# Performance work log

Hardware: AMD Instinct MI355X
Metric: run time of the kernel (lower is better)

## Reference

```python
import jax, jax.numpy as jnp
import numpy as np

B = 1 << 20
N_FREQS = 6          # sin+cos -> 3*2*6 = 36 dims for position
N_BINS = 4           # one-blob bins -> 4 dims per scalar
W_SCALE = 0.18       # ~ sqrt(2/64) He init for ReLU


def freq_embed(p):
    # p: [B,3] -> [B, 3*2*N_FREQS] NeRF-style sin/cos frequency encoding
    freqs = (2.0 ** jnp.arange(N_FREQS, dtype=p.dtype)) * jnp.pi  # [F]
    ang = p[:, :, None] * freqs  # [B,3,F]
    return jnp.concatenate([jnp.sin(ang), jnp.cos(ang)], axis=-1).reshape(p.shape[0], -1)


def one_blob_embed(x):
    # x: [B,D] values in [0,1] -> [B, D*N_BINS] Gaussian one-blob encoding
    centers = (jnp.arange(N_BINS, dtype=x.dtype) + 0.5) / N_BINS  # [K]
    sigma = 1.0 / N_BINS
    val = jnp.exp(-0.5 * ((x[:, :, None] - centers) / sigma) ** 2)  # [B,D,K]
    return val.reshape(x.shape[0], -1)


def to_sphe_coords(d):
    # unit direction [B,3] -> normalized (theta, phi) in [0,1]^2
    theta = jnp.arccos(jnp.clip(d[:, 2], -1.0, 1.0)) / jnp.pi
    phi = jnp.arctan2(d[:, 1], d[:, 0]) / (2.0 * jnp.pi) + 0.5
    return jnp.stack([theta, phi], axis=-1)


def setup_inputs() -> dict:
    key = jax.random.key(0)
    ks = jax.random.split(key, 13)
    p = jax.random.normal(ks[0], (B, 3), dtype=jnp.float32)
    wi = jax.random.normal(ks[1], (B, 3), dtype=jnp.float32)
    wi = wi / jnp.linalg.norm(wi, axis=-1, keepdims=True)
    n = jax.random.normal(ks[2], (B, 3), dtype=jnp.float32)
    n = n / jnp.linalg.norm(n, axis=-1, keepdims=True)
    alpha = jax.random.uniform(ks[3], (B, 3), dtype=jnp.float32)
    beta = jax.random.uniform(ks[4], (B, 3), dtype=jnp.float32)
    r = jax.random.uniform(ks[5], (B, 1), dtype=jnp.float32)
    Ws = {}
    for i in range(6):
        Ws[f"W{i}"] = jax.random.normal(ks[6 + i], (64, 64), dtype=jnp.float32) * W_SCALE
    Ws["W6"] = jax.random.normal(ks[12], (3, 64), dtype=jnp.float32) * W_SCALE
    return dict(p=p, wi=wi, n=n, alpha=alpha, beta=beta, r=r, **Ws)


def reference(p, wi, n, alpha, beta, r, W0, W1, W2, W3, W4, W5, W6):
    x = jnp.concatenate([
        freq_embed(p),                               # 36
        one_blob_embed(to_sphe_coords(wi)),          # 8
        one_blob_embed(to_sphe_coords(n)),           # 8
        one_blob_embed(1.0 - jnp.exp(-r)),           # 4
        alpha,                                       # 3
        beta,                                        # 3
        jnp.ones_like(p[:, :2]),                     # 2 (implicit bias)
    ], axis=-1)  # [B,64]
    h = x
    for W in (W0, W1, W2, W3, W4, W5):
        h = jax.nn.relu(h @ W.T)
    out = h @ W6.T  # [B,3]
    return out * (alpha + beta)  # reflectance factorization
```

## Files before the change

kernel.cpp:

```cpp
#include <hip/hip_runtime.h>

typedef __attribute__((ext_vector_type(8))) short short8;
typedef __attribute__((ext_vector_type(4))) float f32x4;

typedef __attribute__((address_space(3))) unsigned short lds_us;
typedef const __attribute__((address_space(1))) unsigned short glb_us;

__device__ __forceinline__ unsigned short f2bf(float x) {
  union { float f; unsigned u; } v; v.f = x;
  unsigned r = v.u + 0x7fffu + ((v.u >> 16) & 1u);
  return (unsigned short)(r >> 16);
}

#if __has_builtin(__builtin_amdgcn_cvt_pk_bf16_f32)
__device__ __forceinline__ unsigned pk2(float a, float b) {
  return __builtin_bit_cast(unsigned, __builtin_amdgcn_cvt_pk_bf16_f32(a, b));
}
#else
__device__ __forceinline__ unsigned pk2(float a, float b) {
  union { float f; unsigned u; } x, y; x.f = a; y.f = b;
  return __builtin_amdgcn_perm(y.u + 0x8000u, x.u + 0x8000u, 0x07060302u);
}
#endif

__device__ __forceinline__ unsigned relu_pk(unsigned x) {
  unsigned r;
  asm("v_pk_max_i16 %0, %1, %2" : "=v"(r) : "v"(x), "v"(0));
  return r;
}

__device__ __forceinline__ short8 u2s8(uint4 u) {
  union { uint4 a; short8 b; } c; c.a = u; return c.b;
}

__device__ __forceinline__ void wave_mem_fence() {
  asm volatile("" ::: "memory");
  __builtin_amdgcn_wave_barrier();
  asm volatile("" ::: "memory");
}

__device__ __forceinline__ void gload16(const unsigned short* g, unsigned short* l) {
  __builtin_amdgcn_global_load_lds((glb_us*)g, (lds_us*)l, 16, 0, 0);
}

__device__ __forceinline__ float acos01(float z) {
  float ax = fminf(fabsf(z), 1.0f);
  float t  = __builtin_amdgcn_sqrtf(1.0f - ax);
  float p  = fmaf(ax, fmaf(ax, fmaf(ax, -0.00596110f, 0.02363618f),
                           -0.06751692f), 0.49998766f);
  p *= t;
  return z >= 0.0f ? p : 1.0f - p;
}

__device__ __forceinline__ float atan2_01(float y, float x) {
  float ax = fabsf(x), ay = fabsf(y);
  float hi = fmaxf(ax, ay), lo = fminf(ax, ay);
  float r  = lo * __builtin_amdgcn_rcpf(fmaxf(hi, 1e-30f));
  float r2 = r * r;
  float p  = fmaf(r2, fmaf(r2, fmaf(r2, fmaf(r2, fmaf(r2,
               -0.0018655370f, 0.0083800422f), -0.018531250f),
                0.030803547f), -0.052940457f), 0.159151323f);
  float q  = r * p;
  q = (ay > ax) ? 0.25f - q : q;
  q = (x < 0.0f) ? 0.5f - q : q;
  return 0.5f + ((y >= 0.0f) ? q : -q);
}

__device__ __forceinline__ uint2 blob4pk(float x) {
  float x4 = x * 4.0f;
  float e0, e1, e2, e3;
  { float t = x4 - 0.5f; e0 = __builtin_amdgcn_exp2f(t * t * -0.72134752f); }
  { float t = x4 - 1.5f; e1 = __builtin_amdgcn_exp2f(t * t * -0.72134752f); }
  { float t = x4 - 2.5f; e2 = __builtin_amdgcn_exp2f(t * t * -0.72134752f); }
  { float t = x4 - 3.5f; e3 = __builtin_amdgcn_exp2f(t * t * -0.72134752f); }
  return make_uint2(pk2(e0, e1), pk2(e2, e3));
}

__device__ __forceinline__ void freq6(float p, float* s, float* c) {
  float fr = __builtin_amdgcn_fractf(0.5f * p);
  float sv = __builtin_amdgcn_sinf(fr);
  float cv = __builtin_amdgcn_cosf(fr);
  s[0] = sv; c[0] = cv;
#pragma unroll
  for (int i = 1; i < 6; ++i) {
    float t  = sv * cv;
    float ss = sv * sv;
    sv = t + t;
    cv = 1.0f - (ss + ss);
    s[i] = sv; c[i] = cv;
  }
}

__global__ void prep_weights(
    const float* __restrict__ W0, const float* __restrict__ W1,
    const float* __restrict__ W2, const float* __restrict__ W3,
    const float* __restrict__ W4, const float* __restrict__ W5,
    const float* __restrict__ W6, unsigned short* __restrict__ wb)
{
  int idx = blockIdx.x * blockDim.x + threadIdx.x;
  if (idx < 24576) {
    int l = idx >> 12;
    const float* W = (l==0)?W0:(l==1)?W1:(l==2)?W2:(l==3)?W3:(l==4)?W4:W5;
    int j   = idx & 7;
    int ln  = (idx >> 3) & 63;
    int h   = (idx >> 9) & 1;
    int t   = (idx >> 10) & 3;
    int n15 = ln & 15, q = ln >> 4;
    int src = 32*(t>>1) + 8*(n15>>2) + 4*(t&1) + (n15&3);
    int col = h*32 + q*8 + j;
    wb[idx] = f2bf(W[src*64 + col]);
  } else if (idx < 25600) {
    int i6  = idx - 24576;
    int j   = i6 & 7;
    int ln  = (i6 >> 3) & 63;
    int h   = (i6 >> 9) & 1;
    int n15 = ln & 15, q = ln >> 4;
    wb[idx] = (n15 < 3) ? f2bf(W6[n15*64 + h*32 + q*8 + j]) : (unsigned short)0;
  }
}

__global__ __launch_bounds__(256, 4) void nrc_mlp(
    const float* __restrict__ P, const float* __restrict__ WI,
    const float* __restrict__ NRM, const float* __restrict__ ALPHA,
    const float* __restrict__ BETA, const float* __restrict__ R,
    const unsigned short* __restrict__ wb, float* __restrict__ out)
{
  __shared__ __align__(16) unsigned short lds[20480];
  unsigned short* Wb = lds;
  const int lane = threadIdx.x & 63;
  const int wv   = threadIdx.x >> 6;
  unsigned short* Xw = lds + 4096 + (wv << 12);
  const int n15 = lane & 15;
  const int q   = lane >> 4;
  const int row0 = (blockIdx.x * 4 + wv) * 64;
  const int l16 = lane * 8;

  {
    int c0 = 2*wv*512;
    gload16(wb + c0 + l16,        Wb + c0 + l16);
    gload16(wb + c0 + 512 + l16,  Wb + c0 + 512 + l16);
  }

  {
    const int row = row0 + lane;
    const int sw  = lane & 7;
    unsigned short* xr = Xw + (lane << 6);
#define XST(j) (*(uint4*)(xr + (((j) ^ sw) << 3)))

    float s0[6], c0[6], s1[6], c1[6], s2[6], c2[6];
    freq6(P[row*3+0], s0, c0);
    freq6(P[row*3+1], s1, c1);
    freq6(P[row*3+2], s2, c2);

    XST(0) = make_uint4(pk2(s0[0],s0[1]), pk2(s0[2],s0[3]),
                        pk2(s0[4],s0[5]), pk2(c0[0],c0[1]));
    XST(1) = make_uint4(pk2(c0[2],c0[3]), pk2(c0[4],c0[5]),
                        pk2(s1[0],s1[1]), pk2(s1[2],s1[3]));
    XST(2) = make_uint4(pk2(s1[4],s1[5]), pk2(c1[0],c1[1]),
                        pk2(c1[2],c1[3]), pk2(c1[4],c1[5]));
    XST(3) = make_uint4(pk2(s2[0],s2[1]), pk2(s2[2],s2[3]),
                        pk2(s2[4],s2[5]), pk2(c2[0],c2[1]));

    uint2 bwt, bwp, bnt, bnp, brr;
    {
      float wx = WI[row*3+0], wy = WI[row*3+1], wz = WI[row*3+2];
      bwt = blob4pk(acos01(wz));
      bwp = blob4pk(atan2_01(wy, wx));
    }
    {
      float nx = NRM[row*3+0], ny = NRM[row*3+1], nz = NRM[row*3+2];
      bnt = blob4pk(acos01(nz));
      bnp = blob4pk(atan2_01(ny, nx));
    }
    brr = blob4pk(1.0f - __builtin_amdgcn_exp2f(R[row] * -1.44269504f));

    XST(4) = make_uint4(pk2(c2[2],c2[3]), pk2(c2[4],c2[5]), bwt.x, bwt.y);
    XST(5) = make_uint4(bwp.x, bwp.y, bnt.x, bnt.y);
    XST(6) = make_uint4(bnp.x, bnp.y, brr.x, brr.y);

    float a0 = ALPHA[row*3+0], a1 = ALPHA[row*3+1], a2 = ALPHA[row*3+2];
    float e0 = BETA[row*3+0],  e1 = BETA[row*3+1],  e2 = BETA[row*3+2];
    XST(7) = make_uint4(pk2(a0,a1), pk2(a2,e0), pk2(e1,e2), 0x3F803F80u);
#undef XST
  }
  wave_mem_fence();

  uint4 b0[4], b1[4];
  {
    const int swr = n15 & 7;
#pragma unroll
    for (int g = 0; g < 4; ++g) {
      const unsigned short* rb = Xw + ((g*16 + n15) << 6);
      b0[g] = *(const uint4*)(rb + (((q    ) ^ swr) << 3));
      b1[g] = *(const uint4*)(rb + (((q + 4) ^ swr) << 3));
    }
  }

  __syncthreads();

  const f32x4 z = {0.f, 0.f, 0.f, 0.f};

#pragma unroll
  for (int l = 0; l < 6; ++l) {
    short8 a0[4], a1[4];
#pragma unroll
    for (int t = 0; t < 4; ++t) {
      a0[t] = *(const short8*)(Wb + t*1024 + l16);
      a1[t] = *(const short8*)(Wb + t*1024 + 512 + l16);
    }
    __syncthreads();

    if (l < 5) {
      int ns = (l+1) * 4096;
      int c0 = 2*wv*512;
      gload16(wb + ns + c0 + l16,       Wb + c0 + l16);
      gload16(wb + ns + c0 + 512 + l16, Wb + c0 + 512 + l16);
    } else if (wv < 2) {
      int c0 = wv*512;
      gload16(wb + 24576 + c0 + l16, Wb + c0 + l16);
    }

    f32x4 acc[4][4];
#pragma unroll
    for (int t = 0; t < 4; ++t) {
#pragma unroll
      for (int g = 0; g < 4; ++g) {
        f32x4 c = __builtin_amdgcn_mfma_f32_16x16x32_bf16(a0[t], u2s8(b0[g]), z, 0, 0, 0);
        acc[g][t] = __builtin_amdgcn_mfma_f32_16x16x32_bf16(a1[t], u2s8(b1[g]), c, 0, 0, 0);
      }
    }

#pragma unroll
    for (int g = 0; g < 4; ++g) {
      uint4 n0, n1;
      n0.x = relu_pk(pk2(acc[g][0][0], acc[g][0][1]));
      n0.y = relu_pk(pk2(acc[g][0][2], acc[g][0][3]));
      n0.z = relu_pk(pk2(acc[g][1][0], acc[g][1][1]));
      n0.w = relu_pk(pk2(acc[g][1][2], acc[g][1][3]));
      n1.x = relu_pk(pk2(acc[g][2][0], acc[g][2][1]));
      n1.y = relu_pk(pk2(acc[g][2][2], acc[g][2][3]));
      n1.z = relu_pk(pk2(acc[g][3][0], acc[g][3][1]));
      n1.w = relu_pk(pk2(acc[g][3][2], acc[g][3][3]));
      b0[g] = n0; b1[g] = n1;
    }
    __syncthreads();
  }

  {
    short8 o0 = *(const short8*)(Wb + l16);
    short8 o1 = *(const short8*)(Wb + 512 + l16);
#pragma unroll
    for (int g = 0; g < 4; ++g) {
      f32x4 c = __builtin_amdgcn_mfma_f32_16x16x32_bf16(o0, u2s8(b0[g]), z, 0, 0, 0);
      c       = __builtin_amdgcn_mfma_f32_16x16x32_bf16(o1, u2s8(b1[g]), c, 0, 0, 0);
      if (q == 0) {
        int base = row0*3 + g*48 + n15*3;
        float3 av = *(const float3*)(ALPHA + base);
        float3 bv = *(const float3*)(BETA + base);
        float3 o;
        o.x = c[0] * (av.x + bv.x);
        o.y = c[1] * (av.y + bv.y);
        o.z = c[2] * (av.z + bv.z);
        *(float3*)(out + base) = o;
      }
    }
  }
}

extern "C" void kernel_launch(void* const* d_in, const int* in_sizes, int n_in,
                              void* d_out, int out_size, void* d_ws, size_t ws_size,
                              hipStream_t stream) {
  const float* P  = (const float*)d_in[0];
  const float* WI = (const float*)d_in[1];
  const float* NR = (const float*)d_in[2];
  const float* AL = (const float*)d_in[3];
  const float* BE = (const float*)d_in[4];
  const float* R  = (const float*)d_in[5];
  const float* W0 = (const float*)d_in[6];
  const float* W1 = (const float*)d_in[7];
  const float* W2 = (const float*)d_in[8];
  const float* W3 = (const float*)d_in[9];
  const float* W4 = (const float*)d_in[10];
  const float* W5 = (const float*)d_in[11];
  const float* W6 = (const float*)d_in[12];
  unsigned short* wb = (unsigned short*)d_ws;
  float* out = (float*)d_out;

  prep_weights<<<100, 256, 0, stream>>>(W0, W1, W2, W3, W4, W5, W6, wb);
  nrc_mlp<<<4096, 256, 0, stream>>>(P, WI, NR, AL, BE, R, wb, out);
}
```

Baseline: 160.5 us.

## Make MLP kernel persistent with all weights resident in LDS and prefetched inputs

Each block now loads all seven layers' bf16 weights into LDS once and loops over eight 256-row tiles, so per-layer weight streaming and the block-wide barriers between layers go away. The next tile's inputs are loaded from global memory during the current tile's MLP, and the encode stage writes through a smaller, padded per-wave staging buffer in two halves. The grid shrinks from 4096 to 512 blocks and launch bounds fall to two blocks per CU, trading occupancy and latency hiding for amortised weight loads and fewer syncs.

```diff
diff --git a/kernel.cpp b/kernel.cpp
--- a/kernel.cpp
+++ b/kernel.cpp
@@ -119,151 +119,160 @@
   }
 }
 
-__global__ __launch_bounds__(256, 4) void nrc_mlp(
+struct Enc {
+  float p0,p1,p2, wx,wy,wz, nx,ny,nz, a0,a1,a2, e0,e1,e2, rr;
+};
+
+__device__ __forceinline__ Enc load_inputs(
+    const float* __restrict__ P, const float* __restrict__ WI,
+    const float* __restrict__ NRM, const float* __restrict__ ALPHA,
+    const float* __restrict__ BETA, const float* __restrict__ R, int row)
+{
+  Enc v;
+  v.p0 = P[row*3+0];  v.p1 = P[row*3+1];  v.p2 = P[row*3+2];
+  v.wx = WI[row*3+0]; v.wy = WI[row*3+1]; v.wz = WI[row*3+2];
+  v.nx = NRM[row*3+0]; v.ny = NRM[row*3+1]; v.nz = NRM[row*3+2];
+  v.a0 = ALPHA[row*3+0]; v.a1 = ALPHA[row*3+1]; v.a2 = ALPHA[row*3+2];
+  v.e0 = BETA[row*3+0];  v.e1 = BETA[row*3+1];  v.e2 = BETA[row*3+2];
+  v.rr = R[row];
+  return v;
+}
+
+__device__ __forceinline__ void encode_stage(
+    const Enc& v, unsigned short* __restrict__ Xw,
+    int lane, int n15, int q, uint4* b0, uint4* b1)
+{
+  unsigned short* xr = Xw + lane*40;
+
+  float s0[6], c0[6], s1[6], c1[6], s2[6], c2[6];
+  freq6(v.p0, s0, c0);
+  freq6(v.p1, s1, c1);
+  freq6(v.p2, s2, c2);
+
+  *(uint4*)(xr +  0) = make_uint4(pk2(s0[0],s0[1]), pk2(s0[2],s0[3]),
+                                  pk2(s0[4],s0[5]), pk2(c0[0],c0[1]));
+  *(uint4*)(xr +  8) = make_uint4(pk2(c0[2],c0[3]), pk2(c0[4],c0[5]),
+                                  pk2(s1[0],s1[1]), pk2(s1[2],s1[3]));
+  *(uint4*)(xr + 16) = make_uint4(pk2(s1[4],s1[5]), pk2(c1[0],c1[1]),
+                                  pk2(c1[2],c1[3]), pk2(c1[4],c1[5]));
+  *(uint4*)(xr + 24) = make_uint4(pk2(s2[0],s2[1]), pk2(s2[2],s2[3]),
+                                  pk2(s2[4],s2[5]), pk2(c2[0],c2[1]));
+  wave_mem_fence();
+#pragma unroll
+  for (int g = 0; g < 4; ++g)
+    b0[g] = *(const uint4*)(Xw + (g*16 + n15)*40 + q*8);
+  wave_mem_fence();
+
+  uint2 bwt = blob4pk(acos01(v.wz));
+  uint2 bwp = blob4pk(atan2_01(v.wy, v.wx));
+  uint2 bnt = blob4pk(acos01(v.nz));
+  uint2 bnp = blob4pk(atan2_01(v.ny, v.nx));
+  uint2 brr = blob4pk(1.0f - __builtin_amdgcn_exp2f(v.rr * -1.44269504f));
+
+  *(uint4*)(xr +  0) = make_uint4(pk2(c2[2],c2[3]), pk2(c2[4],c2[5]),
+                                  bwt.x, bwt.y);
+  *(uint4*)(xr +  8) = make_uint4(bwp.x, bwp.y, bnt.x, bnt.y);
+  *(uint4*)(xr + 16) = make_uint4(bnp.x, bnp.y, brr.x, brr.y);
+  *(uint4*)(xr + 24) = make_uint4(pk2(v.a0,v.a1), pk2(v.a2,v.e0),
+                                  pk2(v.e1,v.e2), 0x3F803F80u);
+  wave_mem_fence();
+#pragma unroll
+  for (int g = 0; g < 4; ++g)
+    b1[g] = *(const uint4*)(Xw + (g*16 + n15)*40 + q*8);
+  wave_mem_fence();
+}
+
+__global__ __launch_bounds__(256, 2) void nrc_mlp(
     const float* __restrict__ P, const float* __restrict__ WI,
     const float* __restrict__ NRM, const float* __restrict__ ALPHA,
     const float* __restrict__ BETA, const float* __restrict__ R,
     const unsigned short* __restrict__ wb, float* __restrict__ out)
 {
-  __shared__ __align__(16) unsigned short lds[20480];
-  unsigned short* Wb = lds;
+  __shared__ __align__(16) unsigned short lds[35840];
   const int lane = threadIdx.x & 63;
   const int wv   = threadIdx.x >> 6;
-  unsigned short* Xw = lds + 4096 + (wv << 12);
-  const int n15 = lane & 15;
-  const int q   = lane >> 4;
-  const int row0 = (blockIdx.x * 4 + wv) * 64;
-  const int l16 = lane * 8;
-
-  {
-    int c0 = 2*wv*512;
-    gload16(wb + c0 + l16,        Wb + c0 + l16);
-    gload16(wb + c0 + 512 + l16,  Wb + c0 + 512 + l16);
-  }
-
-  {
-    const int row = row0 + lane;
-    const int sw  = lane & 7;
-    unsigned short* xr = Xw + (lane << 6);
-#define XST(j) (*(uint4*)(xr + (((j) ^ sw) << 3)))
-
-    float s0[6], c0[6], s1[6], c1[6], s2[6], c2[6];
-    freq6(P[row*3+0], s0, c0);
-    freq6(P[row*3+1], s1, c1);
-    freq6(P[row*3+2], s2, c2);
-
-    XST(0) = make_uint4(pk2(s0[0],s0[1]), pk2(s0[2],s0[3]),
-                        pk2(s0[4],s0[5]), pk2(c0[0],c0[1]));
-    XST(1) = make_uint4(pk2(c0[2],c0[3]), pk2(c0[4],c0[5]),
-                        pk2(s1[0],s1[1]), pk2(s1[2],s1[3]));
-    XST(2) = make_uint4(pk2(s1[4],s1[5]), pk2(c1[0],c1[1]),
-                        pk2(c1[2],c1[3]), pk2(c1[4],c1[5]));
-    XST(3) = make_uint4(pk2(s2[0],s2[1]), pk2(s2[2],s2[3]),
-                        pk2(s2[4],s2[5]), pk2(c2[0],c2[1]));
-
-    uint2 bwt, bwp, bnt, bnp, brr;
-    {
-      float wx = WI[row*3+0], wy = WI[row*3+1], wz = WI[row*3+2];
-      bwt = blob4pk(acos01(wz));
-      bwp = blob4pk(atan2_01(wy, wx));
-    }
-    {
-      float nx = NRM[row*3+0], ny = NRM[row*3+1], nz = NRM[row*3+2];
-      bnt = blob4pk(acos01(nz));
-      bnp = blob4pk(atan2_01(ny, nx));
-    }
-    brr = blob4pk(1.0f - __builtin_amdgcn_exp2f(R[row] * -1.44269504f));
-
-    XST(4) = make_uint4(pk2(c2[2],c2[3]), pk2(c2[4],c2[5]), bwt.x, bwt.y);
-    XST(5) = make_uint4(bwp.x, bwp.y, bnt.x, bnt.y);
-    XST(6) = make_uint4(bnp.x, bnp.y, brr.x, brr.y);
-
-    float a0 = ALPHA[row*3+0], a1 = ALPHA[row*3+1], a2 = ALPHA[row*3+2];
-    float e0 = BETA[row*3+0],  e1 = BETA[row*3+1],  e2 = BETA[row*3+2];
-    XST(7) = make_uint4(pk2(a0,a1), pk2(a2,e0), pk2(e1,e2), 0x3F803F80u);
-#undef XST
-  }
-  wave_mem_fence();
+  const int n15  = lane & 15;
+  const int q    = lane >> 4;
+  const int l16  = lane * 8;
+  unsigned short* Xw = lds + 25600 + wv*2560;
+  const int blkrow = blockIdx.x * 2048;
+
+  Enc iv = load_inputs(P, WI, NRM, ALPHA, BETA, R, blkrow + wv*64 + lane);
+
+  for (int c = wv; c < 50; c += 4)
+    gload16(wb + c*512 + l16, lds + c*512 + l16);
 
   uint4 b0[4], b1[4];
-  {
-    const int swr = n15 & 7;
-#pragma unroll
-    for (int g = 0; g < 4; ++g) {
-      const unsigned short* rb = Xw + ((g*16 + n15) << 6);
-      b0[g] = *(const uint4*)(rb + (((q    ) ^ swr) << 3));
-      b1[g] = *(const uint4*)(rb + (((q + 4) ^ swr) << 3));
-    }
-  }
+  encode_stage(iv, Xw, lane, n15, q, b0, b1);
 
   __syncthreads();
 
   const f32x4 z = {0.f, 0.f, 0.f, 0.f};
 
-#pragma unroll
-  for (int l = 0; l < 6; ++l) {
-    short8 a0[4], a1[4];
-#pragma unroll
-    for (int t = 0; t < 4; ++t) {
-      a0[t] = *(const short8*)(Wb + t*1024 + l16);
-      a1[t] = *(const short8*)(Wb + t*1024 + 512 + l16);
-    }
-    __syncthreads();
-
-    if (l < 5) {
-      int ns = (l+1) * 4096;
-      int c0 = 2*wv*512;
-      gload16(wb + ns + c0 + l16,       Wb + c0 + l16);
-      gload16(wb + ns + c0 + 512 + l16, Wb + c0 + 512 + l16);
-    } else if (wv < 2) {
-      int c0 = wv*512;
-      gload16(wb + 24576 + c0 + l16, Wb + c0 + l16);
-    }
-
-    f32x4 acc[4][4];
-#pragma unroll
-    for (int t = 0; t < 4; ++t) {
+#pragma unroll 1
+  for (int t = 0; t < 8; ++t) {
+    Enc ivn;
+    if (t < 7)
+      ivn = load_inputs(P, WI, NRM, ALPHA, BETA, R,
+                        blkrow + (t+1)*256 + wv*64 + lane);
+
+#pragma unroll
+    for (int l = 0; l < 6; ++l) {
+      const unsigned short* Wl = lds + l*4096;
+      short8 a0[4], a1[4];
+#pragma unroll
+      for (int k = 0; k < 4; ++k) {
+        a0[k] = *(const short8*)(Wl + k*1024 + l16);
+        a1[k] = *(const short8*)(Wl + k*1024 + 512 + l16);
+      }
+      f32x4 acc[4][4];
+#pragma unroll
+      for (int k = 0; k < 4; ++k) {
+#pragma unroll
+        for (int g = 0; g < 4; ++g) {
+          f32x4 c = __builtin_amdgcn_mfma_f32_16x16x32_bf16(a0[k], u2s8(b0[g]), z, 0, 0, 0);
+          acc[g][k] = __builtin_amdgcn_mfma_f32_16x16x32_bf16(a1[k], u2s8(b1[g]), c, 0, 0, 0);
+        }
+      }
 #pragma unroll
       for (int g = 0; g < 4; ++g) {
-        f32x4 c = __builtin_amdgcn_mfma_f32_16x16x32_bf16(a0[t], u2s8(b0[g]), z, 0, 0, 0);
-        acc[g][t] = __builtin_amdgcn_mfma_f32_16x16x32_bf16(a1[t], u2s8(b1[g]), c, 0, 0, 0);
+        uint4 n0, n1;
+        n0.x = relu_pk(pk2(acc[g][0][0], acc[g][0][1]));
+        n0.y = relu_pk(pk2(acc[g][0][2], acc[g][0][3]));
+        n0.z = relu_pk(pk2(acc[g][1][0], acc[g][1][1]));
+        n0.w = relu_pk(pk2(acc[g][1][2], acc[g][1][3]));
+        n1.x = relu_pk(pk2(acc[g][2][0], acc[g][2][1]));
+        n1.y = relu_pk(pk2(acc[g][2][2], acc[g][2][3]));
+        n1.z = relu_pk(pk2(acc[g][3][0], acc[g][3][1]));
+        n1.w = relu_pk(pk2(acc[g][3][2], acc[g][3][3]));
+        b0[g] = n0; b1[g] = n1;
       }
     }
 
-#pragma unroll
-    for (int g = 0; g < 4; ++g) {
-      uint4 n0, n1;
-      n0.x = relu_pk(pk2(acc[g][0][0], acc[g][0][1]));
-      n0.y = relu_pk(pk2(acc[g][0][2], acc[g][0][3]));
-      n0.z = relu_pk(pk2(acc[g][1][0], acc[g][1][1]));
-      n0.w = relu_pk(pk2(acc[g][1][2], acc[g][1][3]));
-      n1.x = relu_pk(pk2(acc[g][2][0], acc[g][2][1]));
-      n1.y = relu_pk(pk2(acc[g][2][2], acc[g][2][3]));
-      n1.z = relu_pk(pk2(acc[g][3][0], acc[g][3][1]));
-      n1.w = relu_pk(pk2(acc[g][3][2], acc[g][3][3]));
-      b0[g] = n0; b1[g] = n1;
-    }
-    __syncthreads();
-  }
-
-  {
-    short8 o0 = *(const short8*)(Wb + l16);
-    short8 o1 = *(const short8*)(Wb + 512 + l16);
-#pragma unroll
-    for (int g = 0; g < 4; ++g) {
-      f32x4 c = __builtin_amdgcn_mfma_f32_16x16x32_bf16(o0, u2s8(b0[g]), z, 0, 0, 0);
-      c       = __builtin_amdgcn_mfma_f32_16x16x32_bf16(o1, u2s8(b1[g]), c, 0, 0, 0);
-      if (q == 0) {
-        int base = row0*3 + g*48 + n15*3;
-        float3 av = *(const float3*)(ALPHA + base);
-        float3 bv = *(const float3*)(BETA + base);
-        float3 o;
-        o.x = c[0] * (av.x + bv.x);
-        o.y = c[1] * (av.y + bv.y);
-        o.z = c[2] * (av.z + bv.z);
-        *(float3*)(out + base) = o;
+    {
+      const unsigned short* W6l = lds + 24576;
+      short8 o0 = *(const short8*)(W6l + l16);
+      short8 o1 = *(const short8*)(W6l + 512 + l16);
+      const int row0 = blkrow + t*256 + wv*64;
+#pragma unroll
+      for (int g = 0; g < 4; ++g) {
+        f32x4 c = __builtin_amdgcn_mfma_f32_16x16x32_bf16(o0, u2s8(b0[g]), z, 0, 0, 0);
+        c       = __builtin_amdgcn_mfma_f32_16x16x32_bf16(o1, u2s8(b1[g]), c, 0, 0, 0);
+        if (q == 0) {
+          int base = row0*3 + g*48 + n15*3;
+          float3 av = *(const float3*)(ALPHA + base);
+          float3 bv = *(const float3*)(BETA + base);
+          float3 o;
+          o.x = c[0] * (av.x + bv.x);
+          o.y = c[1] * (av.y + bv.y);
+          o.z = c[2] * (av.z + bv.z);
+          *(float3*)(out + base) = o;
+        }
       }
     }
+
+    if (t < 7)
+      encode_stage(ivn, Xw, lane, n15, q, b0, b1);
   }
 }
 
@@ -287,5 +296,5 @@
   float* out = (float*)d_out;
 
   prep_weights<<<100, 256, 0, stream>>>(W0, W1, W2, W3, W4, W5, W6, wb);
-  nrc_mlp<<<4096, 256, 0, stream>>>(P, WI, NR, AL, BE, R, wb, out);
-}
+  nrc_mlp<<<512, 256, 0, stream>>>(P, WI, NR, AL, BE, R, wb, out);
+}
```

Result: slower. 166.4 us (+3.6%).

## Double-buffer per-layer MLP weights in LDS to drop a barrier per layer

Applied to the files above, without the earlier changes.

Adds a second LDS weight buffer so the next layer's weights are prefetched into the alternate buffer while the current layer reads its own. This removes the barrier that used to sit between reading the current layer's weights and starting the next prefetch, so global weight loads overlap with MFMA work. In exchange, per-block LDS grows from 40KB to 48KB and the launch-bounds occupancy hint drops from 4 to 3 blocks per CU, which lowers latency hiding from concurrent blocks.

```diff
diff --git a/kernel.cpp b/kernel.cpp
--- a/kernel.cpp
+++ b/kernel.cpp
@@ -119,26 +119,25 @@
   }
 }
 
-__global__ __launch_bounds__(256, 4) void nrc_mlp(
+__global__ __launch_bounds__(256, 3) void nrc_mlp(
     const float* __restrict__ P, const float* __restrict__ WI,
     const float* __restrict__ NRM, const float* __restrict__ ALPHA,
     const float* __restrict__ BETA, const float* __restrict__ R,
     const unsigned short* __restrict__ wb, float* __restrict__ out)
 {
-  __shared__ __align__(16) unsigned short lds[20480];
-  unsigned short* Wb = lds;
+  __shared__ __align__(16) unsigned short lds[24576];
   const int lane = threadIdx.x & 63;
   const int wv   = threadIdx.x >> 6;
-  unsigned short* Xw = lds + 4096 + (wv << 12);
-  const int n15 = lane & 15;
-  const int q   = lane >> 4;
+  const int n15  = lane & 15;
+  const int q    = lane >> 4;
+  const int l16  = lane * 8;
+  unsigned short* Xw = lds + 8192 + (wv << 12);
   const int row0 = (blockIdx.x * 4 + wv) * 64;
-  const int l16 = lane * 8;
 
   {
     int c0 = 2*wv*512;
-    gload16(wb + c0 + l16,        Wb + c0 + l16);
-    gload16(wb + c0 + 512 + l16,  Wb + c0 + 512 + l16);
+    gload16(wb + c0 + l16,        lds + c0 + l16);
+    gload16(wb + c0 + 512 + l16,  lds + c0 + 512 + l16);
   }
 
   {
@@ -202,31 +201,32 @@
 
 #pragma unroll
   for (int l = 0; l < 6; ++l) {
-    short8 a0[4], a1[4];
-#pragma unroll
-    for (int t = 0; t < 4; ++t) {
-      a0[t] = *(const short8*)(Wb + t*1024 + l16);
-      a1[t] = *(const short8*)(Wb + t*1024 + 512 + l16);
-    }
-    __syncthreads();
-
     if (l < 5) {
+      unsigned short* nb = lds + ((l+1) & 1) * 4096;
       int ns = (l+1) * 4096;
       int c0 = 2*wv*512;
-      gload16(wb + ns + c0 + l16,       Wb + c0 + l16);
-      gload16(wb + ns + c0 + 512 + l16, Wb + c0 + 512 + l16);
+      gload16(wb + ns + c0 + l16,       nb + c0 + l16);
+      gload16(wb + ns + c0 + 512 + l16, nb + c0 + 512 + l16);
     } else if (wv < 2) {
       int c0 = wv*512;
-      gload16(wb + 24576 + c0 + l16, Wb + c0 + l16);
+      gload16(wb + 24576 + c0 + l16, lds + c0 + l16);
+    }
+
+    const unsigned short* Wl = lds + (l & 1) * 4096;
+    short8 a0[4], a1[4];
+#pragma unroll
+    for (int k = 0; k < 4; ++k) {
+      a0[k] = *(const short8*)(Wl + k*1024 + l16);
+      a1[k] = *(const short8*)(Wl + k*1024 + 512 + l16);
     }
 
     f32x4 acc[4][4];
 #pragma unroll
-    for (int t = 0; t < 4; ++t) {
+    for (int k = 0; k < 4; ++k) {
 #pragma unroll
       for (int g = 0; g < 4; ++g) {
-        f32x4 c = __builtin_amdgcn_mfma_f32_16x16x32_bf16(a0[t], u2s8(b0[g]), z, 0, 0, 0);
-        acc[g][t] = __builtin_amdgcn_mfma_f32_16x16x32_bf16(a1[t], u2s8(b1[g]), c, 0, 0, 0);
+        f32x4 c = __builtin_amdgcn_mfma_f32_16x16x32_bf16(a0[k], u2s8(b0[g]), z, 0, 0, 0);
+        acc[g][k] = __builtin_amdgcn_mfma_f32_16x16x32_bf16(a1[k], u2s8(b1[g]), c, 0, 0, 0);
       }
     }
 
@@ -247,8 +247,8 @@
   }
 
   {
-    short8 o0 = *(const short8*)(Wb + l16);
-    short8 o1 = *(const short8*)(Wb + 512 + l16);
+    short8 o0 = *(const short8*)(lds + l16);
+    short8 o1 = *(const short8*)(lds + 512 + l16);
 #pragma unroll
     for (int g = 0; g < 4; ++g) {
       f32x4 c = __builtin_amdgcn_mfma_f32_16x16x32_bf16(o0, u2s8(b0[g]), z, 0, 0, 0);
```

Result: slower. 164.2 us (+2.3%).
